# Kernel optimization log

Hardware: AMD Instinct MI355X
Metric: run time of the kernel (lower is better)

The kernel has to match this reference:

```python
import jax, jax.numpy as jnp
import numpy as np

N, E, T, D = 50000, 800000, 400000, 64


def _linear_params(key, fan_in, fan_out):
    kw, kb = jax.random.split(key)
    s = 1.0 / np.sqrt(fan_in)
    W = jax.random.uniform(kw, (fan_in, fan_out), minval=-s, maxval=s, dtype=jnp.float32)
    b = jax.random.uniform(kb, (fan_out,), minval=-s, maxval=s, dtype=jnp.float32)
    return W, b


def setup_inputs() -> dict:
    key = jax.random.key(0)
    ks = jax.random.split(key, 11)
    Ws1, bs1 = _linear_params(ks[0], 2 * D, D)
    Ws2, bs2 = _linear_params(ks[1], D, 3 * D)
    Wc1, bc1 = _linear_params(ks[2], 2 * D, D)
    Wc2, bc2 = _linear_params(ks[3], D, D)
    WV, bV = _linear_params(ks[4], D, D)
    return {
        "node_scalar": jax.random.normal(ks[5], (N, D), dtype=jnp.float32),
        "node_chiral": jax.random.normal(ks[6], (N, D), dtype=jnp.float32),
        "node_vector": jax.random.normal(ks[7], (N, 3, D), dtype=jnp.float32),
        "pos": jax.random.normal(ks[8], (N, 3), dtype=jnp.float32),
        "edge_index": jax.random.randint(ks[9], (E, 2), 0, N, dtype=jnp.int64),
        "triplet_index": jax.random.randint(ks[10], (T, 4), 0, N, dtype=jnp.int64),
        "Ws1": Ws1, "bs1": bs1, "Ws2": Ws2, "bs2": bs2,
        "Wc1": Wc1, "bc1": bc1, "Wc2": Wc2, "bc2": bc2,
        "WV": WV, "bV": bV,
    }


def reference(node_scalar, node_chiral, node_vector, pos, edge_index, triplet_index,
              Ws1, bs1, Ws2, bs2, Wc1, bc1, Wc2, bc2, WV, bV):
    n = node_scalar.shape[0]
    d = node_scalar.shape[1]
    e0, e1 = edge_index[:, 0], edge_index[:, 1]

    # Scalar / vector section: gather -> Linear-SiLU-Linear gate -> scatter-add
    g = jax.nn.silu(jnp.concatenate([node_scalar[e0], node_scalar[e1]], axis=1) @ Ws1 + bs1) @ Ws2 + bs2
    gate_vector, gate_edge, messages_ss = jnp.split(g, 3, axis=1)  # each [E, d]
    messages_vv = gate_vector[:, None, :] * node_vector[e1]               # [E, 3, d]
    rel = pos[e1] - pos[e0]                                               # [E, 3]
    messages_ev = gate_edge[:, None, :] * rel[:, :, None]                 # [E, 3, d]
    msg_ss = jax.ops.segment_sum(messages_ss, e0, num_segments=n)
    msg_vv = jax.ops.segment_sum(messages_vv, e0, num_segments=n)
    msg_ev = jax.ops.segment_sum(messages_ev, e0, num_segments=n)

    Vv = node_vector @ WV + bV          # [N, 3, d]
    Vv_norm = jnp.linalg.norm(Vv, axis=1)  # [N, d] (norm over spatial axis)
    message_vs = node_scalar * Vv_norm

    # Chiral section: triplet gathers, shared gate MLP, scalar triple product
    base, t1, t2, t3 = (triplet_index[:, i] for i in range(4))
    hc_base = node_chiral[base]

    def cgate(other):
        h = jnp.concatenate([hc_base, node_chiral[other]], axis=1)
        return jax.nn.silu(h @ Wc1 + bc1) @ Wc2 + bc2

    chiral_gate = cgate(t1) + cgate(t2) + cgate(t3)  # [T, d]
    pb = pos[base]
    r1, r2, r3 = pb - pos[t1], pb - pos[t2], pb - pos[t3]
    stp = jnp.einsum('ei,ei->e', r1, jnp.cross(r2, r3))  # scalar triple product [T]
    chiral_messages = chiral_gate / (stp + 0.01)[:, None]
    msg_chiral = jax.ops.segment_sum(chiral_messages, base, num_segments=n)

    return (node_scalar + msg_ss + message_vs,
            node_chiral + msg_chiral,
            node_vector + msg_vv + msg_ev)
```

## Files before the change

### kernel.cpp

```cpp
#include <hip/hip_runtime.h>
#include <math.h>

#define DD 64
typedef unsigned short ushort_t;

__device__ __forceinline__ float silu_f(float x) {
    return x / (1.0f + __expf(-x));
}

__device__ __forceinline__ unsigned f32_to_bf16_rne(float x) {
    unsigned u = __float_as_uint(x);
    unsigned r = ((u >> 16) & 1u) + 0x7fffu;
    return (u + r) >> 16;
}

__device__ __forceinline__ float bf16_to_f32(ushort_t v) {
    return __uint_as_float(((unsigned)v) << 16);
}

__device__ __forceinline__ float2 bf2_lo_hi(unsigned u) {
    return make_float2(__uint_as_float(u << 16), __uint_as_float(u & 0xffff0000u));
}

__device__ __forceinline__ void gload_lds4(const void* gsrc, void* lds_base) {
    __builtin_amdgcn_global_load_lds(
        (const __attribute__((address_space(1))) void*)gsrc,
        (__attribute__((address_space(3))) void*)lds_base,
        4, 0, 0);
}

#define RFL(x) __builtin_amdgcn_readfirstlane(x)

__global__ __launch_bounds__(256) void node_transform_kernel(
    const float* __restrict__ ns, const float* __restrict__ nc,
    const float* __restrict__ Ws1, const float* __restrict__ Wc1,
    ushort_t* __restrict__ Abf, ushort_t* __restrict__ Bbf,
    float* __restrict__ C, float* __restrict__ Dm,
    float* __restrict__ out1, int N)
{
    __shared__ float w1[128 * 64];
    __shared__ float wc1s[128 * 64];
    __shared__ float xs[4][2][64];
    __shared__ float ys[4][2][64];
    int tid = threadIdx.x;
    for (int i = tid; i < 128 * 64 / 4; i += 256) {
        ((float4*)w1)[i]   = ((const float4*)Ws1)[i];
        ((float4*)wc1s)[i] = ((const float4*)Wc1)[i];
    }
    __syncthreads();
    int wave = tid >> 6, lane = tid & 63;
    for (int nb = blockIdx.x * 8; nb < N; nb += gridDim.x * 8) {
        int n0 = nb + wave * 2;
        #pragma unroll
        for (int s = 0; s < 2; ++s) {
            int n = n0 + s;
            float xv = 0.f, yv = 0.f;
            if (n < N) { xv = ns[(size_t)n * DD + lane]; yv = nc[(size_t)n * DD + lane]; }
            xs[wave][s][lane] = xv;
            ys[wave][s][lane] = yv;
        }
        float aA[2] = {0.f, 0.f}, aB[2] = {0.f, 0.f}, aC[2] = {0.f, 0.f}, aD[2] = {0.f, 0.f};
        for (int k = 0; k < 64; ++k) {
            float wa  = w1[k * 64 + lane];
            float wb  = w1[(64 + k) * 64 + lane];
            float wca = wc1s[k * 64 + lane];
            float wcb = wc1s[(64 + k) * 64 + lane];
            #pragma unroll
            for (int s = 0; s < 2; ++s) {
                float xk = xs[wave][s][k];
                float yk = ys[wave][s][k];
                aA[s] += xk * wa;  aB[s] += xk * wb;
                aC[s] += yk * wca; aD[s] += yk * wcb;
            }
        }
        #pragma unroll
        for (int s = 0; s < 2; ++s) {
            int n = n0 + s;
            if (n < N) {
                Abf[(size_t)n * DD + lane] = (ushort_t)f32_to_bf16_rne(aA[s]);
                Bbf[(size_t)n * DD + lane] = (ushort_t)f32_to_bf16_rne(aB[s]);
                C[(size_t)n * DD + lane]  = aC[s];
                Dm[(size_t)n * DD + lane] = aD[s];
                out1[(size_t)n * DD + lane] = ys[wave][s][lane];
            }
        }
    }
}

__global__ __launch_bounds__(256) void node_vector_kernel(
    const float* __restrict__ ns, const float* __restrict__ nv,
    const float* __restrict__ WV, const float* __restrict__ bV,
    float* __restrict__ out0, float* __restrict__ out2,
    ushort_t* __restrict__ nvbf, int N)
{
    __shared__ float wv[64 * 64];
    __shared__ float vs[4][2][3][64];
    int tid = threadIdx.x;
    for (int i = tid; i < 64 * 64 / 4; i += 256)
        ((float4*)wv)[i] = ((const float4*)WV)[i];
    __syncthreads();
    int wave = tid >> 6, lane = tid & 63;
    float bVj = bV[lane];
    for (int nb = blockIdx.x * 8; nb < N; nb += gridDim.x * 8) {
        int n0 = nb + wave * 2;
        #pragma unroll
        for (int s = 0; s < 2; ++s) {
            int n = n0 + s;
            float v0 = 0.f, v1 = 0.f, v2 = 0.f;
            if (n < N) {
                v0 = nv[((size_t)n * 3 + 0) * DD + lane];
                v1 = nv[((size_t)n * 3 + 1) * DD + lane];
                v2 = nv[((size_t)n * 3 + 2) * DD + lane];
            }
            vs[wave][s][0][lane] = v0; vs[wave][s][1][lane] = v1; vs[wave][s][2][lane] = v2;
        }
        float a0[2], a1[2], a2[2];
        #pragma unroll
        for (int s = 0; s < 2; ++s) { a0[s] = bVj; a1[s] = bVj; a2[s] = bVj; }
        for (int k = 0; k < 64; ++k) {
            float w = wv[k * 64 + lane];
            #pragma unroll
            for (int s = 0; s < 2; ++s) {
                a0[s] += vs[wave][s][0][k] * w;
                a1[s] += vs[wave][s][1][k] * w;
                a2[s] += vs[wave][s][2][k] * w;
            }
        }
        #pragma unroll
        for (int s = 0; s < 2; ++s) {
            int n = n0 + s;
            if (n < N) {
                float norm = sqrtf(a0[s] * a0[s] + a1[s] * a1[s] + a2[s] * a2[s]);
                float x = ns[(size_t)n * DD + lane];
                out0[(size_t)n * DD + lane] = x * (1.f + norm);
                float v0 = vs[wave][s][0][lane], v1 = vs[wave][s][1][lane], v2 = vs[wave][s][2][lane];
                out2[((size_t)n * 3 + 0) * DD + lane] = v0;
                out2[((size_t)n * 3 + 1) * DD + lane] = v1;
                out2[((size_t)n * 3 + 2) * DD + lane] = v2;
                nvbf[((size_t)n * 3 + 0) * DD + lane] = (ushort_t)f32_to_bf16_rne(v0);
                nvbf[((size_t)n * 3 + 1) * DD + lane] = (ushort_t)f32_to_bf16_rne(v1);
                nvbf[((size_t)n * 3 + 2) * DD + lane] = (ushort_t)f32_to_bf16_rne(v2);
            }
        }
    }
}

#define EPW 8
__global__ __launch_bounds__(256) void edge_kernel(
    const ushort_t* __restrict__ Abf, const ushort_t* __restrict__ Bbf,
    const ushort_t* __restrict__ nvbf, const float* __restrict__ pos,
    const int* __restrict__ eidx,
    const float* __restrict__ bs1, const float* __restrict__ Ws2, const float* __restrict__ bs2,
    float* __restrict__ out0, float* __restrict__ out2, int E)
{
    __shared__ unsigned w2p[32 * 192];
    __shared__ ushort_t stAB[4][EPW][128];
    __shared__ ushort_t stNV01[4][EPW][128];
    __shared__ ushort_t stNV2[4][EPW / 2][128];
    __shared__ float    stH[4][EPW][64];
    int tid = threadIdx.x;
    for (int i = tid; i < 32 * 192; i += 256) {
        int kp = i / 192, c = i % 192;
        float a = Ws2[(size_t)(2 * kp) * 192 + c];
        float b = Ws2[(size_t)(2 * kp + 1) * 192 + c];
        w2p[i] = f32_to_bf16_rne(a) | (f32_to_bf16_rne(b) << 16);
    }
    __syncthreads();
    int wave = RFL(tid >> 6);
    int lane = tid & 63;
    float b1  = bs1[lane];
    float b2v = bs2[lane], b2e = bs2[64 + lane], b2s = bs2[128 + lane];

    long nG = ((long)E + EPW - 1) / EPW;
    for (long g = (long)blockIdx.x * 4 + wave; g < nG; g += (long)gridDim.x * 4) {
        long e0b = g * EPW;
        int i0a[EPW], i1a[EPW];
        #pragma unroll
        for (int e = 0; e < EPW; ++e) {
            long eid = e0b + e; if (eid >= E) eid = E - 1;
            int2 p = ((const int2*)eidx)[eid];
            i0a[e] = RFL(p.x);
            i1a[e] = RFL(p.y);
        }
        #pragma unroll
        for (int e = 0; e < EPW; ++e) {
            const char* srcAB = (lane < 32)
                ? ((const char*)Abf + (size_t)i0a[e] * 128 + lane * 4)
                : ((const char*)Bbf + (size_t)i1a[e] * 128 + (lane - 32) * 4);
            gload_lds4(srcAB, &stAB[wave][e][0]);
            gload_lds4((const char*)nvbf + (size_t)i1a[e] * 384 + lane * 4, &stNV01[wave][e][0]);
        }
        #pragma unroll
        for (int p = 0; p < EPW / 2; ++p) {
            const char* src2 = (lane < 32)
                ? ((const char*)nvbf + (size_t)i1a[2 * p] * 384 + 256 + lane * 4)
                : ((const char*)nvbf + (size_t)i1a[2 * p + 1] * 384 + 256 + (lane - 32) * 4);
            gload_lds4(src2, &stNV2[wave][p][0]);
        }
        asm volatile("s_waitcnt vmcnt(0)" ::: "memory");
        #pragma unroll
        for (int e = 0; e < EPW; ++e) {
            float a = bf16_to_f32(stAB[wave][e][lane]);
            float b = bf16_to_f32(stAB[wave][e][64 + lane]);
            stH[wave][e][lane] = silu_f(a + b + b1);
        }
        float agv[EPW], age[EPW], ass[EPW];
        #pragma unroll
        for (int e = 0; e < EPW; ++e) { agv[e] = b2v; age[e] = b2e; ass[e] = b2s; }
        for (int k4 = 0; k4 < 64; k4 += 4) {
            int kp = k4 >> 1;
            float2 w0a = bf2_lo_hi(w2p[kp * 192 + lane]);
            float2 w0b = bf2_lo_hi(w2p[(kp + 1) * 192 + lane]);
            float2 w1a = bf2_lo_hi(w2p[kp * 192 + 64 + lane]);
            float2 w1b = bf2_lo_hi(w2p[(kp + 1) * 192 + 64 + lane]);
            float2 w2a = bf2_lo_hi(w2p[kp * 192 + 128 + lane]);
            float2 w2b = bf2_lo_hi(w2p[(kp + 1) * 192 + 128 + lane]);
            #pragma unroll
            for (int e = 0; e < EPW; ++e) {
                float4 hk = *(const float4*)&stH[wave][e][k4];
                agv[e] += hk.x * w0a.x + hk.y * w0a.y + hk.z * w0b.x + hk.w * w0b.y;
                age[e] += hk.x * w1a.x + hk.y * w1a.y + hk.z * w1b.x + hk.w * w1b.y;
                ass[e] += hk.x * w2a.x + hk.y * w2a.y + hk.z * w2b.x + hk.w * w2b.y;
            }
        }
        #pragma unroll
        for (int e = 0; e < EPW; ++e) {
            long eid = e0b + e;
            if (eid >= E) break;
            int i0 = i0a[e], i1 = i1a[e];
            float gv = agv[e], ge = age[e];
            unsafeAtomicAdd(&out0[(unsigned)i0 * 64u + lane], ass[e]);
            float rx = pos[(size_t)i1 * 3 + 0] - pos[(size_t)i0 * 3 + 0];
            float ry = pos[(size_t)i1 * 3 + 1] - pos[(size_t)i0 * 3 + 1];
            float rz = pos[(size_t)i1 * 3 + 2] - pos[(size_t)i0 * 3 + 2];
            float v0 = bf16_to_f32(stNV01[wave][e][lane]);
            float v1 = bf16_to_f32(stNV01[wave][e][64 + lane]);
            float v2 = bf16_to_f32(stNV2[wave][e >> 1][(e & 1) * 64 + lane]);
            unsafeAtomicAdd(&out2[((unsigned)i0 * 3u + 0) * 64u + lane], gv * v0 + ge * rx);
            unsafeAtomicAdd(&out2[((unsigned)i0 * 3u + 1) * 64u + lane], gv * v1 + ge * ry);
            unsafeAtomicAdd(&out2[((unsigned)i0 * 3u + 2) * 64u + lane], gv * v2 + ge * rz);
        }
    }
}

#define TPW 4
__global__ __launch_bounds__(256) void triplet_kernel(
    const float* __restrict__ C, const float* __restrict__ Dm,
    const float* __restrict__ pos, const int* __restrict__ tidx,
    const float* __restrict__ bc1, const float* __restrict__ Wc2, const float* __restrict__ bc2,
    float* __restrict__ out1, int T)
{
    __shared__ float wT[64 * 64];
    __shared__ float stC[4][TPW][64];
    __shared__ float stD[4][TPW][3][64];
    int tid = threadIdx.x;
    for (int i = tid; i < 64 * 64 / 4; i += 256)
        ((float4*)wT)[i] = ((const float4*)Wc2)[i];
    __syncthreads();
    int wave = RFL(tid >> 6);
    int lane = tid & 63;
    float b1 = bc1[lane];
    float b2 = bc2[lane] * 3.0f;
    for (long bb = (long)blockIdx.x * (4 * TPW); bb < T; bb += (long)gridDim.x * (4 * TPW)) {
        long t0 = bb + wave * TPW;
        int ib[TPW], it1[TPW], it2[TPW], it3[TPW];
        #pragma unroll
        for (int e = 0; e < TPW; ++e) {
            long t = t0 + e;
            int b = 0, t1 = 0, t2 = 0, t3 = 0;
            if (t < T) { int4 q = ((const int4*)tidx)[t]; b = q.x; t1 = q.y; t2 = q.z; t3 = q.w; }
            ib[e]  = RFL(b);
            it1[e] = RFL(t1);
            it2[e] = RFL(t2);
            it3[e] = RFL(t3);
        }
        #pragma unroll
        for (int e = 0; e < TPW; ++e) {
            gload_lds4(C  + (size_t)ib[e]  * DD + lane, &stC[wave][e][0]);
            gload_lds4(Dm + (size_t)it1[e] * DD + lane, &stD[wave][e][0][0]);
            gload_lds4(Dm + (size_t)it2[e] * DD + lane, &stD[wave][e][1][0]);
            gload_lds4(Dm + (size_t)it3[e] * DD + lane, &stD[wave][e][2][0]);
        }
        asm volatile("s_waitcnt vmcnt(0)" ::: "memory");
        float inv[TPW];
        #pragma unroll
        for (int e = 0; e < TPW; ++e) {
            float hb = stC[wave][e][lane] + b1;
            float h = silu_f(hb + stD[wave][e][0][lane])
                    + silu_f(hb + stD[wave][e][1][lane])
                    + silu_f(hb + stD[wave][e][2][lane]);
            stC[wave][e][lane] = h;
            int b = ib[e], t1 = it1[e], t2 = it2[e], t3 = it3[e];
            double pbx = pos[(size_t)b * 3], pby = pos[(size_t)b * 3 + 1], pbz = pos[(size_t)b * 3 + 2];
            double r1x = pbx - pos[(size_t)t1 * 3], r1y = pby - pos[(size_t)t1 * 3 + 1], r1z = pbz - pos[(size_t)t1 * 3 + 2];
            double r2x = pbx - pos[(size_t)t2 * 3], r2y = pby - pos[(size_t)t2 * 3 + 1], r2z = pbz - pos[(size_t)t2 * 3 + 2];
            double r3x = pbx - pos[(size_t)t3 * 3], r3y = pby - pos[(size_t)t3 * 3 + 1], r3z = pbz - pos[(size_t)t3 * 3 + 2];
            double cx = r2y * r3z - r2z * r3y;
            double cy = r2z * r3x - r2x * r3z;
            double cz = r2x * r3y - r2y * r3x;
            double stp = r1x * cx + r1y * cy + r1z * cz;
            inv[e] = (float)(1.0 / (stp + 0.01));
        }
        float acc[TPW];
        #pragma unroll
        for (int e = 0; e < TPW; ++e) acc[e] = 0.f;
        for (int k4 = 0; k4 < 64; k4 += 4) {
            float4 hk[TPW];
            #pragma unroll
            for (int e = 0; e < TPW; ++e) hk[e] = *(const float4*)&stC[wave][e][k4];
            #pragma unroll
            for (int kk = 0; kk < 4; ++kk) {
                float wk = wT[(k4 + kk) * 64 + lane];
                #pragma unroll
                for (int e = 0; e < TPW; ++e) acc[e] += (&hk[e].x)[kk] * wk;
            }
        }
        #pragma unroll
        for (int e = 0; e < TPW; ++e) {
            long t = t0 + e;
            if (t >= T) break;
            unsafeAtomicAdd(&out1[(size_t)ib[e] * DD + lane], (acc[e] + b2) * inv[e]);
        }
    }
}

extern "C" void kernel_launch(void* const* d_in, const int* in_sizes, int n_in,
                              void* d_out, int out_size, void* d_ws, size_t ws_size,
                              hipStream_t stream)
{
    const float* ns  = (const float*)d_in[0];
    const float* nc  = (const float*)d_in[1];
    const float* nv  = (const float*)d_in[2];
    const float* pos = (const float*)d_in[3];
    const int* eidx  = (const int*)d_in[4];
    const int* tidx  = (const int*)d_in[5];
    const float* Ws1 = (const float*)d_in[6];
    const float* bs1 = (const float*)d_in[7];
    const float* Ws2 = (const float*)d_in[8];
    const float* bs2 = (const float*)d_in[9];
    const float* Wc1 = (const float*)d_in[10];
    const float* bc1 = (const float*)d_in[11];
    const float* Wc2 = (const float*)d_in[12];
    const float* bc2 = (const float*)d_in[13];
    const float* WV  = (const float*)d_in[14];
    const float* bV  = (const float*)d_in[15];

    int N = in_sizes[0] / 64;
    int E = in_sizes[4] / 2;
    int T = in_sizes[5] / 4;

    float* out0 = (float*)d_out;
    float* out1 = out0 + (size_t)N * 64;
    float* out2 = out1 + (size_t)N * 64;

    float* C  = (float*)d_ws;
    float* Dm = C + (size_t)N * 64;
    ushort_t* Abf  = (ushort_t*)(Dm + (size_t)N * 64);
    ushort_t* Bbf  = Abf + (size_t)N * 64;
    ushort_t* nvbf = Bbf + (size_t)N * 64;

    node_transform_kernel<<<2048, 256, 0, stream>>>(ns, nc, Ws1, Wc1, Abf, Bbf, C, Dm, out1, N);
    node_vector_kernel<<<2048, 256, 0, stream>>>(ns, nv, WV, bV, out0, out2, nvbf, N);
    edge_kernel<<<4096, 256, 0, stream>>>(Abf, Bbf, nvbf, pos, eidx, bs1, Ws2, bs2, out0, out2, E);
    triplet_kernel<<<4096, 256, 0, stream>>>(C, Dm, pos, tidx, bc1, Wc2, bc2, out1, T);
}
```

Measured before the change: 934.4 us.

## Use bf16 MFMA for edge gate second layer and precompute edge displacements

Moves the edge MLP's 64x192 second linear layer from scalar FMA loops onto MFMA 16x16x32 bf16 instructions. Ws2 is pre-swizzled into fragment layout in LDS, and the SiLU hidden values are stored XOR-swizzled in place in the staging buffer. Edges per wave grow from 8 to 16 to fill the MFMA tile. A separate kernel precomputes per-edge relative positions, which are loaded into LDS asynchronously, replacing per-edge pos gathers. This cuts VALU work, but hidden activations are now rounded to bf16 and the atomic scatter order changes.

Result: faster. 914.6 us (-2.1%).

```diff
diff --git a/kernel.cpp b/kernel.cpp
--- a/kernel.cpp
+++ b/kernel.cpp
@@ -3,6 +3,8 @@
 
 #define DD 64
 typedef unsigned short ushort_t;
+typedef __attribute__((ext_vector_type(8))) short bf16x8;
+typedef __attribute__((ext_vector_type(4))) float f32x4;
 
 __device__ __forceinline__ float silu_f(float x) {
     return x / (1.0f + __expf(-x));
@@ -16,10 +18,6 @@
 
 __device__ __forceinline__ float bf16_to_f32(ushort_t v) {
     return __uint_as_float(((unsigned)v) << 16);
-}
-
-__device__ __forceinline__ float2 bf2_lo_hi(unsigned u) {
-    return make_float2(__uint_as_float(u << 16), __uint_as_float(u & 0xffff0000u));
 }
 
 __device__ __forceinline__ void gload_lds4(const void* gsrc, void* lds_base) {
@@ -30,6 +28,19 @@
 }
 
 #define RFL(x) __builtin_amdgcn_readfirstlane(x)
+
+__global__ __launch_bounds__(256) void rel_kernel(const int* __restrict__ eidx,
+                                                  const float* __restrict__ pos,
+                                                  float* __restrict__ relg, int E)
+{
+    int e = blockIdx.x * 256 + threadIdx.x;
+    if (e < E) {
+        int2 p = ((const int2*)eidx)[e];
+        relg[3 * (size_t)e + 0] = pos[(size_t)p.y * 3 + 0] - pos[(size_t)p.x * 3 + 0];
+        relg[3 * (size_t)e + 1] = pos[(size_t)p.y * 3 + 1] - pos[(size_t)p.x * 3 + 1];
+        relg[3 * (size_t)e + 2] = pos[(size_t)p.y * 3 + 2] - pos[(size_t)p.x * 3 + 2];
+    }
+}
 
 __global__ __launch_bounds__(256) void node_transform_kernel(
     const float* __restrict__ ns, const float* __restrict__ nc,
@@ -145,45 +156,57 @@
     }
 }
 
-#define EPW 8
+#define GEPW 16
 __global__ __launch_bounds__(256) void edge_kernel(
     const ushort_t* __restrict__ Abf, const ushort_t* __restrict__ Bbf,
-    const ushort_t* __restrict__ nvbf, const float* __restrict__ pos,
+    const ushort_t* __restrict__ nvbf, const float* __restrict__ relg,
     const int* __restrict__ eidx,
     const float* __restrict__ bs1, const float* __restrict__ Ws2, const float* __restrict__ bs2,
     float* __restrict__ out0, float* __restrict__ out2, int E)
 {
-    __shared__ unsigned w2p[32 * 192];
-    __shared__ ushort_t stAB[4][EPW][128];
-    __shared__ ushort_t stNV01[4][EPW][128];
-    __shared__ ushort_t stNV2[4][EPW / 2][128];
-    __shared__ float    stH[4][EPW][64];
+    __shared__ unsigned w2frag[12 * 2 * 64 * 4];
+    __shared__ ushort_t stAB[4][GEPW][128];
+    __shared__ ushort_t stNV01[4][GEPW][132];
+    __shared__ ushort_t stNV2[4][GEPW / 2][132];
+    __shared__ float    relL[4][64];
     int tid = threadIdx.x;
-    for (int i = tid; i < 32 * 192; i += 256) {
-        int kp = i / 192, c = i % 192;
-        float a = Ws2[(size_t)(2 * kp) * 192 + c];
-        float b = Ws2[(size_t)(2 * kp + 1) * 192 + c];
-        w2p[i] = f32_to_bf16_rne(a) | (f32_to_bf16_rne(b) << 16);
+    for (int i = tid; i < 12 * 2 * 64; i += 256) {
+        int t  = i >> 7;
+        int kk = (i >> 6) & 1;
+        int l  = i & 63;
+        int k0 = kk * 32 + (l >> 4) * 8;
+        int col = t * 16 + (l & 15);
+        #pragma unroll
+        for (int jp = 0; jp < 4; ++jp) {
+            float a = Ws2[(size_t)(k0 + 2 * jp) * 192 + col];
+            float b = Ws2[(size_t)(k0 + 2 * jp + 1) * 192 + col];
+            w2frag[i * 4 + jp] = f32_to_bf16_rne(a) | (f32_to_bf16_rne(b) << 16);
+        }
     }
     __syncthreads();
     int wave = RFL(tid >> 6);
     int lane = tid & 63;
-    float b1  = bs1[lane];
-    float b2v = bs2[lane], b2e = bs2[64 + lane], b2s = bs2[128 + lane];
-
-    long nG = ((long)E + EPW - 1) / EPW;
+    float b1 = bs1[lane];
+    float b2v_t[4], b2e_t[4], b2s_t[4];
+    #pragma unroll
+    for (int t = 0; t < 4; ++t) {
+        b2v_t[t] = bs2[t * 16 + (lane & 15)];
+        b2e_t[t] = bs2[64 + t * 16 + (lane & 15)];
+        b2s_t[t] = bs2[128 + t * 16 + (lane & 15)];
+    }
+
+    long nG = ((long)E + GEPW - 1) / GEPW;
     for (long g = (long)blockIdx.x * 4 + wave; g < nG; g += (long)gridDim.x * 4) {
-        long e0b = g * EPW;
-        int i0a[EPW], i1a[EPW];
-        #pragma unroll
-        for (int e = 0; e < EPW; ++e) {
+        long e0b = g * GEPW;
+        int i0a[GEPW], i1a[GEPW];
+        #pragma unroll
+        for (int e = 0; e < GEPW; ++e) {
             long eid = e0b + e; if (eid >= E) eid = E - 1;
             int2 p = ((const int2*)eidx)[eid];
-            i0a[e] = RFL(p.x);
-            i1a[e] = RFL(p.y);
-        }
-        #pragma unroll
-        for (int e = 0; e < EPW; ++e) {
+            i0a[e] = RFL(p.x); i1a[e] = RFL(p.y);
+        }
+        #pragma unroll
+        for (int e = 0; e < GEPW; ++e) {
             const char* srcAB = (lane < 32)
                 ? ((const char*)Abf + (size_t)i0a[e] * 128 + lane * 4)
                 : ((const char*)Bbf + (size_t)i1a[e] * 128 + (lane - 32) * 4);
@@ -191,54 +214,75 @@
             gload_lds4((const char*)nvbf + (size_t)i1a[e] * 384 + lane * 4, &stNV01[wave][e][0]);
         }
         #pragma unroll
-        for (int p = 0; p < EPW / 2; ++p) {
+        for (int p2 = 0; p2 < GEPW / 2; ++p2) {
             const char* src2 = (lane < 32)
-                ? ((const char*)nvbf + (size_t)i1a[2 * p] * 384 + 256 + lane * 4)
-                : ((const char*)nvbf + (size_t)i1a[2 * p + 1] * 384 + 256 + (lane - 32) * 4);
-            gload_lds4(src2, &stNV2[wave][p][0]);
-        }
+                ? ((const char*)nvbf + (size_t)i1a[2 * p2] * 384 + 256 + lane * 4)
+                : ((const char*)nvbf + (size_t)i1a[2 * p2 + 1] * 384 + 256 + (lane - 32) * 4);
+            gload_lds4(src2, &stNV2[wave][p2][0]);
+        }
+        gload_lds4((const char*)relg + e0b * 12 + lane * 4, &relL[wave][0]);
         asm volatile("s_waitcnt vmcnt(0)" ::: "memory");
-        #pragma unroll
-        for (int e = 0; e < EPW; ++e) {
+        __builtin_amdgcn_sched_barrier(0);
+        #pragma unroll
+        for (int e = 0; e < GEPW; ++e) {
             float a = bf16_to_f32(stAB[wave][e][lane]);
             float b = bf16_to_f32(stAB[wave][e][64 + lane]);
-            stH[wave][e][lane] = silu_f(a + b + b1);
-        }
-        float agv[EPW], age[EPW], ass[EPW];
-        #pragma unroll
-        for (int e = 0; e < EPW; ++e) { agv[e] = b2v; age[e] = b2e; ass[e] = b2s; }
-        for (int k4 = 0; k4 < 64; k4 += 4) {
-            int kp = k4 >> 1;
-            float2 w0a = bf2_lo_hi(w2p[kp * 192 + lane]);
-            float2 w0b = bf2_lo_hi(w2p[(kp + 1) * 192 + lane]);
-            float2 w1a = bf2_lo_hi(w2p[kp * 192 + 64 + lane]);
-            float2 w1b = bf2_lo_hi(w2p[(kp + 1) * 192 + 64 + lane]);
-            float2 w2a = bf2_lo_hi(w2p[kp * 192 + 128 + lane]);
-            float2 w2b = bf2_lo_hi(w2p[(kp + 1) * 192 + 128 + lane]);
-            #pragma unroll
-            for (int e = 0; e < EPW; ++e) {
-                float4 hk = *(const float4*)&stH[wave][e][k4];
-                agv[e] += hk.x * w0a.x + hk.y * w0a.y + hk.z * w0b.x + hk.w * w0b.y;
-                age[e] += hk.x * w1a.x + hk.y * w1a.y + hk.z * w1b.x + hk.w * w1b.y;
-                ass[e] += hk.x * w2a.x + hk.y * w2a.y + hk.z * w2b.x + hk.w * w2b.y;
-            }
-        }
-        #pragma unroll
-        for (int e = 0; e < EPW; ++e) {
-            long eid = e0b + e;
-            if (eid >= E) break;
-            int i0 = i0a[e], i1 = i1a[e];
-            float gv = agv[e], ge = age[e];
-            unsafeAtomicAdd(&out0[(unsigned)i0 * 64u + lane], ass[e]);
-            float rx = pos[(size_t)i1 * 3 + 0] - pos[(size_t)i0 * 3 + 0];
-            float ry = pos[(size_t)i1 * 3 + 1] - pos[(size_t)i0 * 3 + 1];
-            float rz = pos[(size_t)i1 * 3 + 2] - pos[(size_t)i0 * 3 + 2];
-            float v0 = bf16_to_f32(stNV01[wave][e][lane]);
-            float v1 = bf16_to_f32(stNV01[wave][e][64 + lane]);
-            float v2 = bf16_to_f32(stNV2[wave][e >> 1][(e & 1) * 64 + lane]);
-            unsafeAtomicAdd(&out2[((unsigned)i0 * 3u + 0) * 64u + lane], gv * v0 + ge * rx);
-            unsafeAtomicAdd(&out2[((unsigned)i0 * 3u + 1) * 64u + lane], gv * v1 + ge * ry);
-            unsafeAtomicAdd(&out2[((unsigned)i0 * 3u + 2) * 64u + lane], gv * v2 + ge * rz);
+            float h = silu_f(a + b + b1);
+            *(float*)((char*)&stAB[wave][e][0] + ((lane * 4) ^ ((e & 7) << 5))) = h;
+        }
+        __builtin_amdgcn_sched_barrier(0);
+        f32x4 acc[12];
+        f32x4 zz = {0.f, 0.f, 0.f, 0.f};
+        #pragma unroll
+        for (int t = 0; t < 12; ++t) acc[t] = zz;
+        int row = lane & 15;
+        #pragma unroll
+        for (int kk = 0; kk < 2; ++kk) {
+            int coff = (kk * 128 + ((lane >> 4) * 32)) ^ ((row & 7) << 5);
+            const char* hp = (const char*)&stAB[wave][row][0] + coff;
+            float4 lo = *(const float4*)hp;
+            float4 hi = *(const float4*)(hp + 16);
+            unsigned a0, a1, a2, a3;
+            asm("v_cvt_pk_bf16_f32 %0, %1, %2" : "=v"(a0) : "v"(lo.x), "v"(lo.y));
+            asm("v_cvt_pk_bf16_f32 %0, %1, %2" : "=v"(a1) : "v"(lo.z), "v"(lo.w));
+            asm("v_cvt_pk_bf16_f32 %0, %1, %2" : "=v"(a2) : "v"(hi.x), "v"(hi.y));
+            asm("v_cvt_pk_bf16_f32 %0, %1, %2" : "=v"(a3) : "v"(hi.z), "v"(hi.w));
+            union { unsigned u[4]; bf16x8 v; } af;
+            af.u[0] = a0; af.u[1] = a1; af.u[2] = a2; af.u[3] = a3;
+            #pragma unroll
+            for (int t = 0; t < 12; ++t) {
+                bf16x8 bf = *(const bf16x8*)&w2frag[((t * 2 + kk) * 64 + lane) * 4];
+                acc[t] = __builtin_amdgcn_mfma_f32_16x16x32_bf16(af.v, bf, acc[t], 0, 0, 0);
+            }
+        }
+        int vi_all = 0;
+        #pragma unroll
+        for (int e = 0; e < GEPW; ++e) vi_all = (lane == e) ? i0a[e] : vi_all;
+        int eLane0 = (lane >> 4) * 4;
+        #pragma unroll
+        for (int rg = 0; rg < 4; ++rg) {
+            int e = eLane0 + rg;
+            int i0 = __builtin_amdgcn_ds_bpermute(e * 4, vi_all);
+            bool ok = (e0b + e) < E;
+            float r0v = relL[wave][e * 3 + 0];
+            float r1v = relL[wave][e * 3 + 1];
+            float r2v = relL[wave][e * 3 + 2];
+            #pragma unroll
+            for (int t = 0; t < 4; ++t) {
+                int dim = t * 16 + (lane & 15);
+                float gv = acc[t][rg]     + b2v_t[t];
+                float ge = acc[4 + t][rg] + b2e_t[t];
+                float ss = acc[8 + t][rg] + b2s_t[t];
+                float v0 = bf16_to_f32(stNV01[wave][e][dim]);
+                float v1 = bf16_to_f32(stNV01[wave][e][64 + dim]);
+                float v2 = bf16_to_f32(stNV2[wave][e >> 1][(e & 1) * 64 + dim]);
+                if (ok) {
+                    unsafeAtomicAdd(&out0[(size_t)(unsigned)i0 * 64u + dim], ss);
+                    unsafeAtomicAdd(&out2[((size_t)(unsigned)i0 * 3u + 0) * 64u + dim], gv * v0 + ge * r0v);
+                    unsafeAtomicAdd(&out2[((size_t)(unsigned)i0 * 3u + 1) * 64u + dim], gv * v1 + ge * r1v);
+                    unsafeAtomicAdd(&out2[((size_t)(unsigned)i0 * 3u + 2) * 64u + dim], gv * v2 + ge * r2v);
+                }
+            }
         }
     }
 }
@@ -353,14 +397,16 @@
     float* out1 = out0 + (size_t)N * 64;
     float* out2 = out1 + (size_t)N * 64;
 
-    float* C  = (float*)d_ws;
-    float* Dm = C + (size_t)N * 64;
-    ushort_t* Abf  = (ushort_t*)(Dm + (size_t)N * 64);
+    float* C    = (float*)d_ws;
+    float* Dm   = C + (size_t)N * 64;
+    float* relg = Dm + (size_t)N * 64;
+    ushort_t* Abf  = (ushort_t*)(relg + (size_t)E * 3 + 64);
     ushort_t* Bbf  = Abf + (size_t)N * 64;
     ushort_t* nvbf = Bbf + (size_t)N * 64;
 
+    rel_kernel<<<(E + 255) / 256, 256, 0, stream>>>(eidx, pos, relg, E);
     node_transform_kernel<<<2048, 256, 0, stream>>>(ns, nc, Ws1, Wc1, Abf, Bbf, C, Dm, out1, N);
     node_vector_kernel<<<2048, 256, 0, stream>>>(ns, nv, WV, bV, out0, out2, nvbf, N);
-    edge_kernel<<<4096, 256, 0, stream>>>(Abf, Bbf, nvbf, pos, eidx, bs1, Ws2, bs2, out0, out2, E);
+    edge_kernel<<<4096, 256, 0, stream>>>(Abf, Bbf, nvbf, relg, eidx, bs1, Ws2, bs2, out0, out2, E);
     triplet_kernel<<<4096, 256, 0, stream>>>(C, Dm, pos, tidx, bc1, Wc2, bc2, out1, T);
 }
```
